# Kernel optimization log

Hardware: AMD Instinct MI355X
Metric: run time of the kernel (lower is better)

## Reference

```python
import jax, jax.numpy as jnp
import numpy as np

K = 8  # search_range in sample_wise_recolor
BIG = 1e30


def setup_inputs() -> dict:
    key = jax.random.key(0)
    ks = jax.random.split(key, 6)
    L, N = 16384, 10000  # L: upsampled candidate voxels (multiple of 8), N: target points
    pred_F = jax.random.normal(ks[0], (L,), jnp.float32)
    cand_xyz = jax.random.normal(ks[1], (L, 3), jnp.float32) * 50.0
    cand_rgb = jax.random.uniform(ks[2], (L, 3), jnp.float32)
    tgt_xyz = jax.random.normal(ks[3], (N, 3), jnp.float32) * 50.0
    tgt_rgb = jax.random.uniform(ks[4], (N, 3), jnp.float32)
    keep_target = jax.random.randint(ks[5], (L,), 0, 2, jnp.int32)
    return {"pred_F": pred_F, "cand_xyz": cand_xyz, "cand_rgb": cand_rgb,
            "tgt_xyz": tgt_xyz, "tgt_rgb": tgt_rgb, "keep_target": keep_target,
            "points_num": 8192}


def _get_keep(pred, points_num):
    # local-max mask over groups of 8 children (scatter of per-row argmax)
    L = pred.shape[0]
    p8 = pred.reshape(-1, 8)
    rows = jnp.arange(p8.shape[0])
    is_local_max = jnp.zeros(p8.shape, dtype=bool).at[rows, jnp.argmax(p8, axis=1)].set(True).reshape(-1)
    # kthvalue over the non-local-max subset: local-max entries pushed to +inf so the
    # k-th smallest of the full sorted array equals the k-th smallest of the subset.
    k = L - points_num  # static python int
    vals = jnp.where(is_local_max, jnp.inf, pred)
    threshold = jnp.sort(vals)[k - 1]
    return (pred > threshold) | is_local_max


def _pairwise_sqdist(a, b):
    # a: [P,3], b: [Q,3] -> [P,Q] squared distances
    a2 = jnp.sum(a * a, axis=1)
    b2 = jnp.sum(b * b, axis=1)
    d2 = a2[:, None] + b2[None, :] - 2.0 * (a @ b.T)
    return jnp.maximum(d2, 0.0)


def _recolor_loss(cand_xyz, rgb, keep, tgt_xyz, tgt_rgb):
    L = cand_xyz.shape[0]
    N = tgt_xyz.shape[0]
    d2 = _pairwise_sqdist(tgt_xyz, cand_xyz)  # [N, L]

    # ---- recolor_backward: KNN from each target point into kept candidates ----
    d_masked = jnp.where(keep[None, :], d2, BIG)
    neg_d, idx = jax.lax.top_k(-d_masked, K)  # [N, K]
    d = -neg_d
    zero_mask = d == 0.0
    min_mask = (d == jnp.min(d, axis=1, keepdims=True)) & ~jnp.any(zero_mask, axis=1)[:, None]
    w = jnp.where(min_mask, 1.0 / jnp.sqrt(jnp.maximum(d, 1e-30)), 0.0)  # [N, K]

    flat_idx = idx.reshape(-1)
    num = jnp.zeros((L, 3), rgb.dtype).at[flat_idx].add((tgt_rgb[:, None, :] * w[:, :, None]).reshape(-1, 3))
    den = jnp.zeros((L,), rgb.dtype).at[flat_idx].add(w.reshape(-1))
    has_den = den != 0.0
    recolored = jnp.where(has_den[:, None], num / jnp.where(has_den, den, 1.0)[:, None], 0.0)

    # exact-match (zero-distance) targets overwrite; scatter with safe out-of-range dummy row
    safe_idx = jnp.where(zero_mask, idx, L).reshape(-1)
    tgt_exp = jnp.broadcast_to(tgt_rgb[:, None, :], (N, K, 3)).reshape(-1, 3)
    recolored = jnp.concatenate([recolored, jnp.zeros((1, 3), rgb.dtype)], 0).at[safe_idx].set(tgt_exp)[:L]
    empty = jnp.concatenate([~has_den, jnp.zeros((1,), bool)], 0).at[safe_idx].set(False)[:L]
    empty = empty & keep  # only kept candidates matter

    # ---- recolor_forward: kept candidates with no color yet pull from nearest targets ----
    neg_df, idxf = jax.lax.top_k(-d2.T, K)  # [L, K]
    df = -neg_df
    mf = df == jnp.min(df, axis=1, keepdims=True)
    rec_fwd = jnp.sum(tgt_rgb[idxf] * mf[:, :, None], axis=1) / jnp.sum(mf, axis=1, keepdims=True).astype(rgb.dtype)
    recolored = jnp.where(empty[:, None], rec_fwd, recolored)

    # L1 loss over kept candidates only; recolor target is no-grad in the original
    recolored = jax.lax.stop_gradient(recolored)
    return jnp.sum(jnp.where(keep[:, None], jnp.abs(rgb - recolored), 0.0))


def reference(pred_F, cand_xyz, cand_rgb, tgt_xyz, tgt_rgb, keep_target, points_num):
    keep = _get_keep(jax.lax.stop_gradient(pred_F), points_num)  # @torch.no_grad
    # coord recon loss: BCE-with-logits, reduction='sum'
    t = keep_target.astype(pred_F.dtype)
    coord_loss = jnp.sum(jnp.maximum(pred_F, 0.0) - pred_F * t + jnp.log1p(jnp.exp(-jnp.abs(pred_F))))
    # inverse_transform_for_color in training mode: x * 255
    rgb = cand_rgb * 255.0
    rgb_loss = _recolor_loss(cand_xyz, rgb, keep, tgt_xyz, tgt_rgb)
    return jnp.stack([coord_loss, rgb_loss])
```

## Files before the change

kernel.cpp:

```cpp
#include <hip/hip_runtime.h>
#include <hip/hip_bf16.h>


#define SCAN_T 256
#define BCH 512
#define FCH 512
typedef unsigned long long ull;

__global__ __launch_bounds__(256) void k_initprep(
    const float* __restrict__ pred, const float* __restrict__ txyz,
    float4* __restrict__ ttile, float4* __restrict__ numden,
    int* __restrict__ zerohit, ull* __restrict__ tmin, ull* __restrict__ fmin,
    unsigned int* __restrict__ key, unsigned char* __restrict__ islm,
    int* __restrict__ counters, float* __restrict__ out, int L, int N) {
  int gidx = blockIdx.x * 256 + threadIdx.x;
  int gsz = (int)gridDim.x * 256;
  for (int i = gidx; i < N; i += gsz) {
    float x = txyz[3*i], y = txyz[3*i+1], z = txyz[3*i+2];
    ttile[i] = make_float4(x, y, z, fmaf(x, x, fmaf(y, y, z * z)));
    tmin[i] = ~0ull;
  }
  for (int i = gidx; i < L; i += gsz) {
    numden[i] = make_float4(0.f, 0.f, 0.f, 0.f);
    zerohit[i] = 0;
    fmin[i] = ~0ull;
  }
  if (gidx < 8) counters[gidx] = 0;
  if (gidx < 2) out[gidx] = 0.f;
  int ngroups = L >> 3;
  for (int g = gidx; g < ngroups; g += gsz) {
    const float4* pv = (const float4*)pred + (size_t)g * 2;
    float4 a = pv[0], b = pv[1];
    float v[8] = {a.x, a.y, a.z, a.w, b.x, b.y, b.z, b.w};
    int bi = 0; float bv = v[0];
    #pragma unroll
    for (int j = 1; j < 8; ++j) if (v[j] > bv) { bv = v[j]; bi = j; }
    unsigned int kk[8];
    ull lmpack = 0ull;
    #pragma unroll
    for (int j = 0; j < 8; ++j) {
      unsigned int fb = __float_as_uint(v[j]);
      unsigned int mk = (fb & 0x80000000u) ? ~fb : (fb | 0x80000000u);
      if (j == bi) { mk = 0xFF800000u; lmpack |= 1ull << (8 * j); }
      kk[j] = mk;
    }
    ((uint4*)key)[g*2]   = make_uint4(kk[0], kk[1], kk[2], kk[3]);
    ((uint4*)key)[g*2+1] = make_uint4(kk[4], kk[5], kk[6], kk[7]);
    *(ull*)(islm + (size_t)g * 8) = lmpack;
  }
}

__device__ __forceinline__ void select_bin(
    unsigned int* hist, int nb, unsigned int rank,
    unsigned int* sB, unsigned int* sR, int tid) {
  if (tid < 64) {
    int g = nb >> 6;
    unsigned int sum = 0;
    for (int j = 0; j < g; ++j) sum += hist[tid * g + j];
    unsigned int incl = sum;
    for (int o = 1; o < 64; o <<= 1) {
      unsigned int v = __shfl_up(incl, o);
      if (tid >= o) incl += v;
    }
    unsigned int excl = incl - sum;
    bool cond = (rank >= excl) && (rank < incl);
    unsigned long long bal = __ballot(cond);
    int first = __ffsll((long long)bal) - 1;
    if (tid == first) {
      unsigned int r = rank - excl, cum = 0;
      for (int j = 0; j < g; ++j) {
        unsigned int c = hist[tid * g + j];
        if (r < cum + c) { *sB = (unsigned int)(tid * g + j); *sR = r - cum; break; }
        cum += c;
      }
    }
  }
}

__global__ __launch_bounds__(256) void k_sel(
    const unsigned int* __restrict__ key, const int* __restrict__ pnum_p,
    float* __restrict__ thr_out, int L) {
  __shared__ unsigned int hist[2048];
  __shared__ unsigned int sB, sR;
  int tid = threadIdx.x;
  unsigned int rank = (unsigned int)(L - pnum_p[0] - 1);
  const uint4* k4 = (const uint4*)key;
  int n4 = L >> 2;
  for (int b = tid; b < 2048; b += 256) hist[b] = 0u;
  __syncthreads();
  for (int i = tid; i < n4; i += 256) {
    uint4 v = k4[i];
    atomicAdd(&hist[v.x >> 21], 1u); atomicAdd(&hist[v.y >> 21], 1u);
    atomicAdd(&hist[v.z >> 21], 1u); atomicAdd(&hist[v.w >> 21], 1u);
  }
  __syncthreads();
  select_bin(hist, 2048, rank, &sB, &sR, tid);
  __syncthreads();
  unsigned int B1 = sB, R1 = sR;
  for (int b = tid; b < 2048; b += 256) hist[b] = 0u;
  __syncthreads();
  for (int i = tid; i < n4; i += 256) {
    uint4 v = k4[i];
    if ((v.x >> 21) == B1) atomicAdd(&hist[(v.x >> 10) & 2047u], 1u);
    if ((v.y >> 21) == B1) atomicAdd(&hist[(v.y >> 10) & 2047u], 1u);
    if ((v.z >> 21) == B1) atomicAdd(&hist[(v.z >> 10) & 2047u], 1u);
    if ((v.w >> 21) == B1) atomicAdd(&hist[(v.w >> 10) & 2047u], 1u);
  }
  __syncthreads();
  select_bin(hist, 2048, R1, &sB, &sR, tid);
  __syncthreads();
  unsigned int B2 = sB, R2 = sR;
  for (int b = tid; b < 1024; b += 256) hist[b] = 0u;
  __syncthreads();
  unsigned int top22 = (B1 << 11) | B2;
  for (int i = tid; i < n4; i += 256) {
    uint4 v = k4[i];
    if ((v.x >> 10) == top22) atomicAdd(&hist[v.x & 1023u], 1u);
    if ((v.y >> 10) == top22) atomicAdd(&hist[v.y & 1023u], 1u);
    if ((v.z >> 10) == top22) atomicAdd(&hist[v.z & 1023u], 1u);
    if ((v.w >> 10) == top22) atomicAdd(&hist[v.w & 1023u], 1u);
  }
  __syncthreads();
  select_bin(hist, 1024, R2, &sB, &sR, tid);
  __syncthreads();
  if (tid == 0) {
    unsigned int fkey = (B1 << 21) | (B2 << 10) | sB;
    unsigned int fb = (fkey & 0x80000000u) ? (fkey & 0x7FFFFFFFu) : ~fkey;
    thr_out[0] = __uint_as_float(fb);
  }
}

__global__ __launch_bounds__(256) void k_keepc(
    const float* __restrict__ pred, const unsigned char* __restrict__ islm,
    const float* __restrict__ thr_p, const float* __restrict__ cxyz,
    const int* __restrict__ ktgt, int* __restrict__ keep,
    float4* __restrict__ klist, int* __restrict__ kidx,
    int* __restrict__ counters, float* __restrict__ out, int L) {
  int i = blockIdx.x * 256 + threadIdx.x;
  float thr = thr_p[0];
  float term = 0.f;
  if (i < L) {
    float p = pred[i];
    bool kp = (p > thr) || islm[i];
    keep[i] = kp ? 1 : 0;
    if (kp) {
      int pos = atomicAdd(&counters[0], 1);
      float x = cxyz[3*i], y = cxyz[3*i+1], z = cxyz[3*i+2];
      klist[pos] = make_float4(x, y, z, fmaf(x, x, fmaf(y, y, z * z)));
      kidx[pos] = i;
    }
    float t = (float)ktgt[i];
    term = fmaxf(p, 0.f) - p * t + log1pf(expf(-fabsf(p)));
  }
  for (int o = 32; o > 0; o >>= 1) term += __shfl_down(term, o);
  if ((threadIdx.x & 63) == 0) atomicAdd(&out[0], term);
}

__global__ __launch_bounds__(SCAN_T) void k_bwd(
    const float* __restrict__ txyz, const float4* __restrict__ klist,
    const int* __restrict__ kidx, const int* __restrict__ counters,
    ull* __restrict__ tmin, int N) {
  int kc = counters[0];
  int c0 = blockIdx.y * BCH;
  if (c0 >= kc) return;
  int c1 = min(c0 + BCH, kc);
  __shared__ float4 sc[SCAN_T];
  int tid = threadIdx.x;
  int t = blockIdx.x * SCAN_T + tid;
  float tx = 0.f, ty = 0.f, tz = 0.f;
  if (t < N) { tx = txyz[3*t]; ty = txyz[3*t+1]; tz = txyz[3*t+2]; }
  float ntx = -2.f * tx, nty = -2.f * ty, ntz = -2.f * tz;
  float best = 3e38f; int bpos = -1;
  for (int tile = c0; tile < c1; tile += SCAN_T) {
    int cnt = min(SCAN_T, c1 - tile);
    if (tid < cnt) sc[tid] = klist[tile + tid];
    __syncthreads();
    #pragma unroll 8
    for (int c = 0; c < cnt; ++c) {
      float4 cd = sc[c];
      float d = fmaf(ntx, cd.x, cd.w);
      d = fmaf(nty, cd.y, d);
      d = fmaf(ntz, cd.z, d);
      if (d < best) { best = d; bpos = tile + c; }
    }
    __syncthreads();
  }
  if (t < N && bpos >= 0) {
    float4 cd = klist[bpos];
    float dx = tx - cd.x, dy = ty - cd.y, dz = tz - cd.z;
    float dtrue = fmaf(dx, dx, fmaf(dy, dy, dz * dz));
    ull pack = ((ull)__float_as_uint(dtrue) << 32) | (unsigned int)kidx[bpos];
    atomicMin(&tmin[t], pack);
  }
}

__global__ __launch_bounds__(256) void k_scatter(
    const float* __restrict__ trgb, const ull* __restrict__ tmin,
    float4* __restrict__ numden, int* __restrict__ zerohit,
    float4* __restrict__ zcolor, int N) {
  int t = blockIdx.x * 256 + threadIdx.x;
  if (t >= N) return;
  ull pack = tmin[t];
  float d = __uint_as_float((unsigned int)(pack >> 32));
  int idx = (int)(pack & 0xFFFFFFFFull);
  float r = trgb[3*t], g = trgb[3*t+1], b = trgb[3*t+2];
  if (d == 0.0f) {
    zerohit[idx] = 1;
    zcolor[idx] = make_float4(r, g, b, 0.f);
  } else {
    float w = 1.0f / sqrtf(fmaxf(d, 1e-30f));
    atomicAdd(&numden[idx].x, r * w);
    atomicAdd(&numden[idx].y, g * w);
    atomicAdd(&numden[idx].z, b * w);
    atomicAdd(&numden[idx].w, w);
  }
}

__global__ __launch_bounds__(256) void k_empty(
    const int* __restrict__ keep, const float4* __restrict__ numden,
    const int* __restrict__ zerohit, int* __restrict__ elist,
    int* __restrict__ counters, int L) {
  int l = blockIdx.x * 256 + threadIdx.x;
  if (l < L && keep[l] && (numden[l].w == 0.f) && (zerohit[l] == 0)) {
    int pos = atomicAdd(&counters[1], 1);
    elist[pos] = l;
  }
}

__global__ __launch_bounds__(SCAN_T) void k_fwd(
    const float4* __restrict__ ttile, const float* __restrict__ cxyz,
    const int* __restrict__ elist, const int* __restrict__ counters,
    ull* __restrict__ fmin, int N) {
  int ec = counters[1];
  if ((int)(blockIdx.x * SCAN_T) >= ec) return;
  __shared__ float4 st[SCAN_T];
  int tid = threadIdx.x;
  int e = blockIdx.x * SCAN_T + tid;
  bool act = e < ec;
  int l = act ? elist[e] : 0;
  float cx = 0.f, cy = 0.f, cz = 0.f;
  if (act) { cx = cxyz[3*l]; cy = cxyz[3*l+1]; cz = cxyz[3*l+2]; }
  float ncx = -2.f * cx, ncy = -2.f * cy, ncz = -2.f * cz;
  float c2 = fmaf(cx, cx, fmaf(cy, cy, cz * cz));
  int t0 = blockIdx.y * FCH;
  int t1 = min(t0 + FCH, N);
  float best = 3e38f; int bidx = 0;
  for (int tile = t0; tile < t1; tile += SCAN_T) {
    int cnt = min(SCAN_T, t1 - tile);
    if (tid < cnt) st[tid] = ttile[tile + tid];
    __syncthreads();
    #pragma unroll 8
    for (int c = 0; c < cnt; ++c) {
      float4 td = st[c];
      float d = fmaf(ncx, td.x, td.w);
      d = fmaf(ncy, td.y, d);
      d = fmaf(ncz, td.z, d);
      if (d < best) { best = d; bidx = tile + c; }
    }
    __syncthreads();
  }
  if (act) {
    float dkey = fmaxf(best + c2, 0.f);
    ull pack = ((ull)__float_as_uint(dkey) << 32) | (unsigned int)bidx;
    atomicMin(&fmin[l], pack);
  }
}

__global__ __launch_bounds__(256) void k_loss(
    const float* __restrict__ crgb, const float* __restrict__ trgb,
    const int* __restrict__ keep, const float4* __restrict__ numden,
    const int* __restrict__ zerohit, const float4* __restrict__ zcolor,
    const ull* __restrict__ fmin, float* __restrict__ out, int L) {
  int l = blockIdx.x * 256 + threadIdx.x;
  float loss = 0.f;
  if (l < L && keep[l]) {
    float rr, rg, rb;
    if (zerohit[l]) {
      float4 z = zcolor[l]; rr = z.x; rg = z.y; rb = z.z;
    } else {
      float4 nd = numden[l];
      if (nd.w != 0.f) { rr = nd.x / nd.w; rg = nd.y / nd.w; rb = nd.z / nd.w; }
      else {
        int ti = (int)(fmin[l] & 0xFFFFFFFFull);
        rr = trgb[3*ti]; rg = trgb[3*ti+1]; rb = trgb[3*ti+2];
      }
    }
    float sr = crgb[3*l]*255.f, sg = crgb[3*l+1]*255.f, sb = crgb[3*l+2]*255.f;
    loss = fabsf(sr - rr) + fabsf(sg - rg) + fabsf(sb - rb);
  }
  for (int o = 32; o > 0; o >>= 1) loss += __shfl_down(loss, o);
  if ((threadIdx.x & 63) == 0) atomicAdd(&out[1], loss);
}

extern "C" void kernel_launch(void* const* d_in, const int* in_sizes, int n_in,
                              void* d_out, int out_size, void* d_ws, size_t ws_size,
                              hipStream_t stream) {
  const float* pred = (const float*)d_in[0];
  const float* cxyz = (const float*)d_in[1];
  const float* crgb = (const float*)d_in[2];
  const float* txyz = (const float*)d_in[3];
  const float* trgb = (const float*)d_in[4];
  const int*   ktgt = (const int*)d_in[5];
  const int*   pnum = (const int*)d_in[6];
  int L = in_sizes[0];
  int N = in_sizes[3] / 3;

  char* ws = (char*)d_ws;
  size_t off = 0;
  float4* klist  = (float4*)(ws + off);   off += (size_t)L * 16;
  float4* ttile  = (float4*)(ws + off);   off += (size_t)((N + 3) & ~3) * 16;
  float4* numden = (float4*)(ws + off);   off += (size_t)L * 16;
  float4* zcolor = (float4*)(ws + off);   off += (size_t)L * 16;
  unsigned int* key = (unsigned int*)(ws + off); off += (size_t)L * 4;
  ull* tmin      = (ull*)(ws + off);      off += (size_t)((N + 1) & ~1) * 8;
  ull* fmin      = (ull*)(ws + off);      off += (size_t)L * 8;
  int* keep      = (int*)(ws + off);      off += (size_t)L * 4;
  int* kidx      = (int*)(ws + off);      off += (size_t)L * 4;
  int* zerohit   = (int*)(ws + off);      off += (size_t)L * 4;
  int* elist     = (int*)(ws + off);      off += (size_t)L * 4;
  float* thr_slot = (float*)(ws + off);   off += 16;
  int* counters  = (int*)(ws + off);      off += 256;
  unsigned char* islm = (unsigned char*)(ws + off); off += ((size_t)L + 15) & ~15ull;
  float* out = (float*)d_out;

  int nbL = (L + 255) / 256;
  int nbN = (N + 255) / 256;
  int mx = max(L, N);

  k_initprep<<<(mx + 255) / 256, 256, 0, stream>>>(
      pred, txyz, ttile, numden, zerohit, tmin, fmin, key, islm, counters, out, L, N);

  k_sel<<<1, 256, 0, stream>>>(key, pnum, thr_slot, L);

  k_keepc<<<nbL, 256, 0, stream>>>(
      pred, islm, thr_slot, cxyz, ktgt, keep, klist, kidx, counters, out, L);

  dim3 g2(nbN, (L + BCH - 1) / BCH);
  k_bwd<<<g2, SCAN_T, 0, stream>>>(txyz, klist, kidx, counters, tmin, N);

  k_scatter<<<nbN, 256, 0, stream>>>(trgb, tmin, numden, zerohit, zcolor, N);

  k_empty<<<nbL, 256, 0, stream>>>(keep, numden, zerohit, elist, counters, L);

  dim3 g3(nbL, (N + FCH - 1) / FCH);
  k_fwd<<<g3, SCAN_T, 0, stream>>>(ttile, cxyz, elist, counters, fmin, N);

  k_loss<<<nbL, 256, 0, stream>>>(
      crgb, trgb, keep, numden, zerohit, zcolor, fmin, out, L);
}
```

Before: 154.8 us.

## Merge backward and forward nearest-neighbor scans into one concurrent launch

The forward scan no longer waits for the backward scan, scatter and empty-list compaction. It now runs speculatively for every kept candidate, and both scans share one 2D grid with the y-blocks split between them. This removes the k_empty kernel, the elist buffer and two serial launch boundaries, so both scans can fill the GPU together. The cost is that forward-scan work is done for all kept candidates, about 8k, instead of only the empty ones. k_loss only reads fmin for candidates with no backward color, so the extra results go unused.

```diff
diff --git a/kernel.cpp b/kernel.cpp
--- a/kernel.cpp
+++ b/kernel.cpp
@@ -3,11 +3,9 @@
 
 
 #define SCAN_T 256
-#define BCH 512
-#define FCH 512
 typedef unsigned long long ull;
 
-__global__ __launch_bounds__(256) void k_initprep(
+__global__ __launch_bounds__(256) void k_prep(
     const float* __restrict__ pred, const float* __restrict__ txyz,
     float4* __restrict__ ttile, float4* __restrict__ numden,
     int* __restrict__ zerohit, ull* __restrict__ tmin, ull* __restrict__ fmin,
@@ -156,41 +154,80 @@
   if ((threadIdx.x & 63) == 0) atomicAdd(&out[0], term);
 }
 
-__global__ __launch_bounds__(SCAN_T) void k_bwd(
+__global__ __launch_bounds__(SCAN_T) void k_scan2(
     const float* __restrict__ txyz, const float4* __restrict__ klist,
-    const int* __restrict__ kidx, const int* __restrict__ counters,
-    ull* __restrict__ tmin, int N) {
+    const int* __restrict__ kidx, const float4* __restrict__ ttile,
+    const int* __restrict__ counters, ull* __restrict__ tmin,
+    ull* __restrict__ fmin, int L, int N, int YB) {
+  __shared__ float4 tile[SCAN_T];
+  int tid = threadIdx.x, x = blockIdx.x, y = blockIdx.y;
   int kc = counters[0];
-  int c0 = blockIdx.y * BCH;
-  if (c0 >= kc) return;
-  int c1 = min(c0 + BCH, kc);
-  __shared__ float4 sc[SCAN_T];
-  int tid = threadIdx.x;
-  int t = blockIdx.x * SCAN_T + tid;
-  float tx = 0.f, ty = 0.f, tz = 0.f;
-  if (t < N) { tx = txyz[3*t]; ty = txyz[3*t+1]; tz = txyz[3*t+2]; }
-  float ntx = -2.f * tx, nty = -2.f * ty, ntz = -2.f * tz;
-  float best = 3e38f; int bpos = -1;
-  for (int tile = c0; tile < c1; tile += SCAN_T) {
-    int cnt = min(SCAN_T, c1 - tile);
-    if (tid < cnt) sc[tid] = klist[tile + tid];
-    __syncthreads();
-    #pragma unroll 8
-    for (int c = 0; c < cnt; ++c) {
-      float4 cd = sc[c];
-      float d = fmaf(ntx, cd.x, cd.w);
-      d = fmaf(nty, cd.y, d);
-      d = fmaf(ntz, cd.z, d);
-      if (d < best) { best = d; bpos = tile + c; }
-    }
-    __syncthreads();
-  }
-  if (t < N && bpos >= 0) {
-    float4 cd = klist[bpos];
-    float dx = tx - cd.x, dy = ty - cd.y, dz = tz - cd.z;
-    float dtrue = fmaf(dx, dx, fmaf(dy, dy, dz * dz));
-    ull pack = ((ull)__float_as_uint(dtrue) << 32) | (unsigned int)kidx[bpos];
-    atomicMin(&tmin[t], pack);
+
+  if (y < YB) {
+    int c0 = y * 512;
+    if (x * 256 >= N || c0 >= kc) return;
+    int c1 = min(c0 + 512, kc);
+    int t = x * 256 + tid;
+    bool act = t < N;
+    float tx = 0.f, ty = 0.f, tz = 0.f;
+    if (act) { tx = txyz[3*t]; ty = txyz[3*t+1]; tz = txyz[3*t+2]; }
+    float ntx = -2.f * tx, nty = -2.f * ty, ntz = -2.f * tz;
+    float best = 3e38f; int bpos = -1;
+    for (int tb = c0; tb < c1; tb += SCAN_T) {
+      int cnt = min(SCAN_T, c1 - tb);
+      if (tid < cnt) tile[tid] = klist[tb + tid];
+      __syncthreads();
+      #pragma unroll 8
+      for (int c = 0; c < cnt; ++c) {
+        float4 cd = tile[c];
+        float d = fmaf(ntx, cd.x, cd.w);
+        d = fmaf(nty, cd.y, d);
+        d = fmaf(ntz, cd.z, d);
+        if (d < best) { best = d; bpos = tb + c; }
+      }
+      __syncthreads();
+    }
+    if (act && bpos >= 0) {
+      float4 cd = klist[bpos];
+      float dx = tx - cd.x, dy = ty - cd.y, dz = tz - cd.z;
+      float dtrue = fmaf(dx, dx, fmaf(dy, dy, dz * dz));
+      ull pack = ((ull)__float_as_uint(dtrue) << 32) | (unsigned int)kidx[bpos];
+      atomicMin(&tmin[t], pack);
+    }
+  } else {
+    int t0 = (y - YB) * 512;
+    if (x * 256 >= kc) return;
+    int t1 = min(t0 + 512, N);
+    int e = x * 256 + tid;
+    bool act = e < kc;
+    float cx = 0.f, cy = 0.f, cz = 0.f, c2 = 0.f;
+    int l = 0;
+    if (act) {
+      float4 cd = klist[e];
+      cx = cd.x; cy = cd.y; cz = cd.z; c2 = cd.w;
+      l = kidx[e];
+    }
+    float ncx = -2.f * cx, ncy = -2.f * cy, ncz = -2.f * cz;
+    float best = 3e38f; int bidx = 0;
+    for (int tb = t0; tb < t1; tb += SCAN_T) {
+      int cnt = min(SCAN_T, t1 - tb);
+      if (tid < cnt) tile[tid] = ttile[tb + tid];
+      __syncthreads();
+      #pragma unroll 8
+      for (int c = 0; c < cnt; ++c) {
+        float4 td = tile[c];
+        float d = fmaf(ncx, td.x, td.w);
+        d = fmaf(ncy, td.y, d);
+        d = fmaf(ncz, td.z, d);
+        if (d < best) { best = d; bidx = tb + c; }
+      }
+      __syncthreads();
+    }
+    if (act) {
+      float dkey = fmaxf(best + c2, 0.f);
+      ull pack = ((ull)__float_as_uint(dkey) << 32) | (unsigned int)bidx;
+      atomicMin(&fmin[l], pack);
+    }
   }
 }
 
@@ -216,56 +253,6 @@
   }
 }
 
-__global__ __launch_bounds__(256) void k_empty(
-    const int* __restrict__ keep, const float4* __restrict__ numden,
-    const int* __restrict__ zerohit, int* __restrict__ elist,
-    int* __restrict__ counters, int L) {
-  int l = blockIdx.x * 256 + threadIdx.x;
-  if (l < L && keep[l] && (numden[l].w == 0.f) && (zerohit[l] == 0)) {
-    int pos = atomicAdd(&counters[1], 1);
-    elist[pos] = l;
-  }
-}
-
-__global__ __launch_bounds__(SCAN_T) void k_fwd(
-    const float4* __restrict__ ttile, const float* __restrict__ cxyz,
-    const int* __restrict__ elist, const int* __restrict__ counters,
-    ull* __restrict__ fmin, int N) {
-  int ec = counters[1];
-  if ((int)(blockIdx.x * SCAN_T) >= ec) return;
-  __shared__ float4 st[SCAN_T];
-  int tid = threadIdx.x;
-  int e = blockIdx.x * SCAN_T + tid;
-  bool act = e < ec;
-  int l = act ? elist[e] : 0;
-  float cx = 0.f, cy = 0.f, cz = 0.f;
-  if (act) { cx = cxyz[3*l]; cy = cxyz[3*l+1]; cz = cxyz[3*l+2]; }
-  float ncx = -2.f * cx, ncy = -2.f * cy, ncz = -2.f * cz;
-  float c2 = fmaf(cx, cx, fmaf(cy, cy, cz * cz));
-  int t0 = blockIdx.y * FCH;
-  int t1 = min(t0 + FCH, N);
-  float best = 3e38f; int bidx = 0;
-  for (int tile = t0; tile < t1; tile += SCAN_T) {
-    int cnt = min(SCAN_T, t1 - tile);
-    if (tid < cnt) st[tid] = ttile[tile + tid];
-    __syncthreads();
-    #pragma unroll 8
-    for (int c = 0; c < cnt; ++c) {
-      float4 td = st[c];
-      float d = fmaf(ncx, td.x, td.w);
-      d = fmaf(ncy, td.y, d);
-      d = fmaf(ncz, td.z, d);
-      if (d < best) { best = d; bidx = tile + c; }
-    }
-    __syncthreads();
-  }
-  if (act) {
-    float dkey = fmaxf(best + c2, 0.f);
-    ull pack = ((ull)__float_as_uint(dkey) << 32) | (unsigned int)bidx;
-    atomicMin(&fmin[l], pack);
-  }
-}
-
 __global__ __launch_bounds__(256) void k_loss(
     const float* __restrict__ crgb, const float* __restrict__ trgb,
     const int* __restrict__ keep, const float4* __restrict__ numden,
@@ -317,7 +304,6 @@
   int* keep      = (int*)(ws + off);      off += (size_t)L * 4;
   int* kidx      = (int*)(ws + off);      off += (size_t)L * 4;
   int* zerohit   = (int*)(ws + off);      off += (size_t)L * 4;
-  int* elist     = (int*)(ws + off);      off += (size_t)L * 4;
   float* thr_slot = (float*)(ws + off);   off += 16;
   int* counters  = (int*)(ws + off);      off += 256;
   unsigned char* islm = (unsigned char*)(ws + off); off += ((size_t)L + 15) & ~15ull;
@@ -325,9 +311,11 @@
 
   int nbL = (L + 255) / 256;
   int nbN = (N + 255) / 256;
+  int YB = (L + 511) / 512;
+  int YF = (N + 511) / 512;
   int mx = max(L, N);
 
-  k_initprep<<<(mx + 255) / 256, 256, 0, stream>>>(
+  k_prep<<<(mx + 255) / 256, 256, 0, stream>>>(
       pred, txyz, ttile, numden, zerohit, tmin, fmin, key, islm, counters, out, L, N);
 
   k_sel<<<1, 256, 0, stream>>>(key, pnum, thr_slot, L);
@@ -335,15 +323,11 @@
   k_keepc<<<nbL, 256, 0, stream>>>(
       pred, islm, thr_slot, cxyz, ktgt, keep, klist, kidx, counters, out, L);
 
-  dim3 g2(nbN, (L + BCH - 1) / BCH);
-  k_bwd<<<g2, SCAN_T, 0, stream>>>(txyz, klist, kidx, counters, tmin, N);
+  dim3 gs(nbL, YB + YF);
+  k_scan2<<<gs, SCAN_T, 0, stream>>>(
+      txyz, klist, kidx, ttile, counters, tmin, fmin, L, N, YB);
 
   k_scatter<<<nbN, 256, 0, stream>>>(trgb, tmin, numden, zerohit, zcolor, N);
-
-  k_empty<<<nbL, 256, 0, stream>>>(keep, numden, zerohit, elist, counters, L);
-
-  dim3 g3(nbL, (N + FCH - 1) / FCH);
-  k_fwd<<<g3, SCAN_T, 0, stream>>>(ttile, cxyz, elist, counters, fmin, N);
 
   k_loss<<<nbL, 256, 0, stream>>>(
       crgb, trgb, keep, numden, zerohit, zcolor, fmin, out, L);
```

New measurement: 140.3 us. -9.4%, faster.
